# Optimization experiments

Measured on AMD Instinct MI355X. Metric: run time of the kernel, lower is better.

The kernel has to match this reference:

```python
import jax, jax.numpy as jnp
import numpy as np

EPS = 1e-6  # flax LayerNorm default

def _layernorm(x, scale, bias):
    mu = jnp.mean(x, axis=-1, keepdims=True)
    var = jnp.mean(jnp.square(x - mu), axis=-1, keepdims=True)
    return (x - mu) * jax.lax.rsqrt(var + EPS) * scale + bias

def _rel_pos_index(ws):
    coords = np.stack(np.meshgrid(np.arange(ws), np.arange(ws), indexing='ij'))  # [2,ws,ws]
    cf = coords.reshape(2, -1)
    rel = (cf[:, :, None] - cf[:, None, :]).transpose(1, 2, 0)  # [N,N,2]
    rel[..., 0] += ws - 1
    rel[..., 1] += ws - 1
    rel[..., 0] *= 2 * ws - 1
    return rel.sum(-1)  # [N,N] in [0,(2ws-1)^2)

def setup_inputs() -> dict:
    key = jax.random.key(0)
    ks = jax.random.split(key, 8)
    B, H, W, C = 16, 56, 56, 384
    L, heads, ws = 2, 12, 7
    s = 0.02
    return {
        'x': jax.random.normal(ks[0], (B, H, W, C), jnp.float32),
        'ln1_s': jnp.ones((L, C), jnp.float32),
        'ln1_b': jnp.zeros((L, C), jnp.float32),
        'qkv_w': jax.random.normal(ks[1], (L, C, 3 * C), jnp.float32) * s,
        'rpb': jax.random.normal(ks[2], (L, (2 * ws - 1) ** 2, heads), jnp.float32) * s,
        'proj_w': jax.random.normal(ks[3], (L, C, C), jnp.float32) * s,
        'ln2_s': jnp.ones((L, C), jnp.float32),
        'ln2_b': jnp.zeros((L, C), jnp.float32),
        'mlp_w1': jax.random.normal(ks[4], (L, C, 4 * C), jnp.float32) * s,
        'mlp_b1': jnp.zeros((L, 4 * C), jnp.float32),
        'mlp_w2': jax.random.normal(ks[5], (L, 4 * C, C), jnp.float32) * s,
        'mlp_b2': jnp.zeros((L, C), jnp.float32),
        'window_size': 7,
    }

def reference(x, ln1_s, ln1_b, qkv_w, rpb, proj_w, ln2_s, ln2_b, mlp_w1, mlp_b1, mlp_w2, mlp_b2, window_size):
    B, H, W, C = x.shape
    ws = int(window_size)
    L = qkv_w.shape[0]
    heads = rpb.shape[-1]
    hd = C // heads
    N = ws * ws
    idx = jnp.asarray(_rel_pos_index(ws))  # [N,N] static

    # --- split to windows: [B,H,W,C] -> [B*nWh*nWw, N, C]
    xw = x.reshape(B, H // ws, ws, W // ws, ws, C)
    xw = xw.transpose(0, 1, 3, 2, 4, 5).reshape(-1, N, C)

    for l in range(L):
        # --- windowed MHSA with relative position bias
        h = _layernorm(xw, ln1_s[l], ln1_b[l])
        qkv = (h @ qkv_w[l]).reshape(-1, N, 3, heads, hd)
        q, k, v = qkv[:, :, 0], qkv[:, :, 1], qkv[:, :, 2]  # [nW,N,heads,hd]
        attn = jnp.einsum('wqhd,wkhd->whqk', q, k) * (hd ** -0.5)
        bias = rpb[l][idx].transpose(2, 0, 1)  # [heads,N,N]
        attn = jax.nn.softmax(attn + bias[None], axis=-1)
        o = jnp.einsum('whqk,wkhd->wqhd', attn, v).reshape(-1, N, C)
        xw = xw + o @ proj_w[l]
        # --- MLP block
        h = _layernorm(xw, ln2_s[l], ln2_b[l])
        h = jax.nn.gelu(h @ mlp_w1[l] + mlp_b1[l])
        xw = xw + (h @ mlp_w2[l] + mlp_b2[l])

    # --- merge windows back to [B,H,W,C]
    out = xw.reshape(B, H // ws, W // ws, ws, ws, C)
    out = out.transpose(0, 1, 3, 2, 4, 5).reshape(B, H, W, C)
    return out
```

## Files before the change

### kernel.cpp

```cpp
#include <hip/hip_runtime.h>
#include <hip/hip_bf16.h>

typedef __bf16 bf16;
typedef __attribute__((ext_vector_type(4))) __bf16 bf16x4;
typedef __attribute__((ext_vector_type(8))) __bf16 bf16x8;
typedef __attribute__((ext_vector_type(4))) float f32x4;

__device__ __forceinline__ void async_ld16(const void* g, void* l) {
    __builtin_amdgcn_global_load_lds(
        (const __attribute__((address_space(1))) unsigned int*)g,
        (__attribute__((address_space(3))) unsigned int*)l, 16, 0, 0);
}

__global__ __launch_bounds__(256) void k_f2bt(const float* __restrict__ in,
                                              bf16* __restrict__ out, int Kd, int Nd) {
    int id = blockIdx.x * 256 + threadIdx.x;
    if (id >= Kd * Nd) return;
    int k = id / Nd, n = id - k * Nd;
    out[(size_t)n * Kd + k] = (bf16)in[id];
}

__global__ __launch_bounds__(256) void k_lnr(const float* __restrict__ x,
                                             const float* __restrict__ s,
                                             const float* __restrict__ b,
                                             float* __restrict__ xres,
                                             bf16* __restrict__ h) {
    int traw = blockIdx.x * 4 + (threadIdx.x >> 6);
    int lane = threadIdx.x & 63;
    int bb = traw / 3136;
    int rem = traw - bb * 3136;
    int y = rem / 56, xc = rem - y * 56;
    int w = bb * 64 + (y / 7) * 8 + (xc / 7);
    int n = (y % 7) * 7 + (xc % 7);
    int twin = w * 49 + n;

    const float4* row = (const float4*)(x + (size_t)traw * 384);
    float4 v0 = row[lane];
    float4 v1 = make_float4(0.f, 0.f, 0.f, 0.f);
    if (lane < 32) v1 = row[64 + lane];
    float sum = v0.x + v0.y + v0.z + v0.w + v1.x + v1.y + v1.z + v1.w;
#pragma unroll
    for (int m = 1; m < 64; m <<= 1) sum += __shfl_xor(sum, m);
    float mu = sum * (1.f / 384.f);
    float sq = (v0.x - mu) * (v0.x - mu) + (v0.y - mu) * (v0.y - mu) +
               (v0.z - mu) * (v0.z - mu) + (v0.w - mu) * (v0.w - mu);
    if (lane < 32)
        sq += (v1.x - mu) * (v1.x - mu) + (v1.y - mu) * (v1.y - mu) +
              (v1.z - mu) * (v1.z - mu) + (v1.w - mu) * (v1.w - mu);
#pragma unroll
    for (int m = 1; m < 64; m <<= 1) sq += __shfl_xor(sq, m);
    float r = rsqrtf(sq * (1.f / 384.f) + 1e-6f);

    float4* xr = (float4*)(xres + (size_t)twin * 384);
    const float4* s4 = (const float4*)s;
    const float4* b4 = (const float4*)b;
    bf16* ho = h + (size_t)twin * 384;
    {
        xr[lane] = v0;
        float4 sv = s4[lane], bv = b4[lane];
        bf16x4 ov;
        ov[0] = (bf16)((v0.x - mu) * r * sv.x + bv.x);
        ov[1] = (bf16)((v0.y - mu) * r * sv.y + bv.y);
        ov[2] = (bf16)((v0.z - mu) * r * sv.z + bv.z);
        ov[3] = (bf16)((v0.w - mu) * r * sv.w + bv.w);
        *(bf16x4*)&ho[lane * 4] = ov;
    }
    if (lane < 32) {
        xr[64 + lane] = v1;
        float4 sv = s4[64 + lane], bv = b4[64 + lane];
        bf16x4 ov;
        ov[0] = (bf16)((v1.x - mu) * r * sv.x + bv.x);
        ov[1] = (bf16)((v1.y - mu) * r * sv.y + bv.y);
        ov[2] = (bf16)((v1.z - mu) * r * sv.z + bv.z);
        ov[3] = (bf16)((v1.w - mu) * r * sv.w + bv.w);
        *(bf16x4*)&ho[256 + lane * 4] = ov;
    }
}

__global__ __launch_bounds__(256) void k_ln(const float* __restrict__ xres,
                                            const float* __restrict__ s,
                                            const float* __restrict__ b,
                                            bf16* __restrict__ h) {
    int t = blockIdx.x * 4 + (threadIdx.x >> 6);
    int lane = threadIdx.x & 63;
    const float4* row = (const float4*)(xres + (size_t)t * 384);
    float4 v0 = row[lane];
    float4 v1 = make_float4(0.f, 0.f, 0.f, 0.f);
    if (lane < 32) v1 = row[64 + lane];
    float sum = v0.x + v0.y + v0.z + v0.w + v1.x + v1.y + v1.z + v1.w;
#pragma unroll
    for (int m = 1; m < 64; m <<= 1) sum += __shfl_xor(sum, m);
    float mu = sum * (1.f / 384.f);
    float sq = (v0.x - mu) * (v0.x - mu) + (v0.y - mu) * (v0.y - mu) +
               (v0.z - mu) * (v0.z - mu) + (v0.w - mu) * (v0.w - mu);
    if (lane < 32)
        sq += (v1.x - mu) * (v1.x - mu) + (v1.y - mu) * (v1.y - mu) +
              (v1.z - mu) * (v1.z - mu) + (v1.w - mu) * (v1.w - mu);
#pragma unroll
    for (int m = 1; m < 64; m <<= 1) sq += __shfl_xor(sq, m);
    float r = rsqrtf(sq * (1.f / 384.f) + 1e-6f);
    const float4* s4 = (const float4*)s;
    const float4* b4 = (const float4*)b;
    bf16* ho = h + (size_t)t * 384;
    {
        float4 sv = s4[lane], bv = b4[lane];
        bf16x4 ov;
        ov[0] = (bf16)((v0.x - mu) * r * sv.x + bv.x);
        ov[1] = (bf16)((v0.y - mu) * r * sv.y + bv.y);
        ov[2] = (bf16)((v0.z - mu) * r * sv.z + bv.z);
        ov[3] = (bf16)((v0.w - mu) * r * sv.w + bv.w);
        *(bf16x4*)&ho[lane * 4] = ov;
    }
    if (lane < 32) {
        float4 sv = s4[64 + lane], bv = b4[64 + lane];
        bf16x4 ov;
        ov[0] = (bf16)((v1.x - mu) * r * sv.x + bv.x);
        ov[1] = (bf16)((v1.y - mu) * r * sv.y + bv.y);
        ov[2] = (bf16)((v1.z - mu) * r * sv.z + bv.z);
        ov[3] = (bf16)((v1.w - mu) * r * sv.w + bv.w);
        *(bf16x4*)&ho[256 + lane * 4] = ov;
    }
}

__device__ inline float gelu_f(float x) {
    float u = 0.7978845608028654f * (x + 0.044715f * x * x * x);
    float t = 1.f - 2.f / (__expf(2.f * u) + 1.f);
    return 0.5f * x * (1.f + t);
}

template <int EPI>
__global__ __launch_bounds__(256) void k_gemm(const bf16* __restrict__ A,
                                              const bf16* __restrict__ Bt,
                                              const float* __restrict__ bias,
                                              float* __restrict__ resid,
                                              bf16* __restrict__ Cout,
                                              float* __restrict__ outf,
                                              int N, int K) {
    __shared__ __align__(16) char lds[17408];
    bf16* As = (bf16*)lds;
    bf16* Bs = (bf16*)(lds + 8192);
    int tid = threadIdx.x;
    int n0 = blockIdx.x * 128;
    int m0 = blockIdx.y * 128;
    int wave = tid >> 6, lane = tid & 63;
    int wm = (wave >> 1) * 64, wn = (wave & 1) * 64;
    int col = lane & 15, quad = lane >> 4;

    f32x4 acc[4][4] = {};

    int r0 = 2 * wave * 16 + (lane >> 2);
    int ksl = (lane & 3) ^ ((r0 >> 1) & 3);
    const bf16* ga0 = A + (size_t)(m0 + r0) * K + ksl * 8;
    const bf16* gb0 = Bt + (size_t)(n0 + r0) * K + ksl * 8;
    size_t rowK16 = (size_t)16 * K;
    bf16* la0 = &As[2 * wave * 512];
    bf16* la1 = &As[(2 * wave + 1) * 512];
    bf16* lb0 = &Bs[2 * wave * 512];
    bf16* lb1 = &Bs[(2 * wave + 1) * 512];

    for (int kb = 0; kb < K; kb += 32) {
        __syncthreads();
        async_ld16(ga0 + kb, la0);
        async_ld16(ga0 + rowK16 + kb, la1);
        async_ld16(gb0 + kb, lb0);
        async_ld16(gb0 + rowK16 + kb, lb1);
        __syncthreads();

        bf16x8 af[4], bfv[4];
#pragma unroll
        for (int i = 0; i < 4; i++) {
            int ra = wm + i * 16 + col;
            af[i] = *(const bf16x8*)&As[ra * 32 + ((quad ^ ((ra >> 1) & 3)) << 3)];
            int rb = wn + i * 16 + col;
            bfv[i] = *(const bf16x8*)&Bs[rb * 32 + ((quad ^ ((rb >> 1) & 3)) << 3)];
        }
#pragma unroll
        for (int mi = 0; mi < 4; mi++)
#pragma unroll
            for (int ni = 0; ni < 4; ni++)
                acc[mi][ni] = __builtin_amdgcn_mfma_f32_16x16x32_bf16(
                    af[mi], bfv[ni], acc[mi][ni], 0, 0, 0);
    }

    __syncthreads();
    float* scrw = (float*)lds + wave * (16 * 68);

    int prow = lane >> 3;
    int pc0 = (lane & 7) * 8;
#pragma unroll
    for (int mi = 0; mi < 4; mi++) {
#pragma unroll
        for (int ni = 0; ni < 4; ni++)
#pragma unroll
            for (int r = 0; r < 4; r++)
                scrw[(quad * 4 + r) * 68 + ni * 16 + col] = acc[mi][ni][r];
#pragma unroll
        for (int h = 0; h < 2; h++) {
            int lr = h * 8 + prow;
            const float* sp = scrw + lr * 68 + pc0;
            float4 u0 = *(const float4*)sp;
            float4 u1 = *(const float4*)(sp + 4);
            int gm = m0 + wm + mi * 16 + lr;
            int gn = n0 + wn + pc0;
            size_t off = (size_t)gm * N + gn;
            if (EPI == 0) {
                bf16x8 ov;
                ov[0] = (bf16)u0.x; ov[1] = (bf16)u0.y; ov[2] = (bf16)u0.z; ov[3] = (bf16)u0.w;
                ov[4] = (bf16)u1.x; ov[5] = (bf16)u1.y; ov[6] = (bf16)u1.z; ov[7] = (bf16)u1.w;
                *(bf16x8*)&Cout[off] = ov;
            } else if (EPI == 1) {
                float4 b0 = *(const float4*)&bias[gn];
                float4 b1 = *(const float4*)&bias[gn + 4];
                bf16x8 ov;
                ov[0] = (bf16)gelu_f(u0.x + b0.x); ov[1] = (bf16)gelu_f(u0.y + b0.y);
                ov[2] = (bf16)gelu_f(u0.z + b0.z); ov[3] = (bf16)gelu_f(u0.w + b0.w);
                ov[4] = (bf16)gelu_f(u1.x + b1.x); ov[5] = (bf16)gelu_f(u1.y + b1.y);
                ov[6] = (bf16)gelu_f(u1.z + b1.z); ov[7] = (bf16)gelu_f(u1.w + b1.w);
                *(bf16x8*)&Cout[off] = ov;
            } else if (EPI == 2) {
                float4 r0v = *(const float4*)&resid[off];
                float4 r1v = *(const float4*)&resid[off + 4];
                r0v.x += u0.x; r0v.y += u0.y; r0v.z += u0.z; r0v.w += u0.w;
                r1v.x += u1.x; r1v.y += u1.y; r1v.z += u1.z; r1v.w += u1.w;
                *(float4*)&resid[off] = r0v;
                *(float4*)&resid[off + 4] = r1v;
            } else if (EPI == 3) {
                float4 b0 = *(const float4*)&bias[gn];
                float4 b1 = *(const float4*)&bias[gn + 4];
                float4 r0v = *(const float4*)&resid[off];
                float4 r1v = *(const float4*)&resid[off + 4];
                r0v.x += u0.x + b0.x; r0v.y += u0.y + b0.y;
                r0v.z += u0.z + b0.z; r0v.w += u0.w + b0.w;
                r1v.x += u1.x + b1.x; r1v.y += u1.y + b1.y;
                r1v.z += u1.z + b1.z; r1v.w += u1.w + b1.w;
                *(float4*)&resid[off] = r0v;
                *(float4*)&resid[off + 4] = r1v;
            } else {
                float4 b0 = *(const float4*)&bias[gn];
                float4 b1 = *(const float4*)&bias[gn + 4];
                float4 r0v = *(const float4*)&resid[off];
                float4 r1v = *(const float4*)&resid[off + 4];
                r0v.x += u0.x + b0.x; r0v.y += u0.y + b0.y;
                r0v.z += u0.z + b0.z; r0v.w += u0.w + b0.w;
                r1v.x += u1.x + b1.x; r1v.y += u1.y + b1.y;
                r1v.z += u1.z + b1.z; r1v.w += u1.w + b1.w;
                int wdx = gm / 49, n = gm - wdx * 49;
                int bb = wdx >> 6, r64 = wdx & 63;
                int n7 = n / 7;
                int yy = (r64 >> 3) * 7 + n7;
                int xx = (r64 & 7) * 7 + (n - n7 * 7);
                size_t traw = ((size_t)((bb * 56 + yy) * 56 + xx)) * 384 + gn;
                *(float4*)&outf[traw] = r0v;
                *(float4*)&outf[traw + 4] = r1v;
            }
        }
    }
}

__global__ __launch_bounds__(256) void k_attn(const bf16* __restrict__ qkv,
                                              const float* __restrict__ rpb,
                                              bf16* __restrict__ o) {
    __shared__ unsigned short relIdx[2401];
    __shared__ float rpbs[4][169];
    __shared__ __align__(16) bf16 Vs[4][32 * 72];
    __shared__ __align__(16) bf16 Ps[4][64 * 72];

    int tid = threadIdx.x;
    int wave = tid >> 6, lane = tid & 63;
    int col = lane & 15, quad = lane >> 4;
    int w = blockIdx.x;
    int head = blockIdx.y * 4 + wave;
    const float scale = 0.17677669529663687f;

    for (int e = tid; e < 2401; e += 256) {
        int i = e / 49, j = e - i * 49;
        int yi = i / 7, xi = i - yi * 7, yj = j / 7, xj = j - yj * 7;
        relIdx[e] = (unsigned short)((yi - yj + 6) * 13 + (xi - xj + 6));
    }
    for (int e = lane; e < 169; e += 64) rpbs[wave][e] = rpb[e * 12 + head];

    const bf16* base = qkv + (size_t)w * 49 * 1152 + head * 32;
    bf16* vsw = Vs[wave];
    bf16* psw = Ps[wave];

    bf16x4 z4 = {(bf16)0.f, (bf16)0.f, (bf16)0.f, (bf16)0.f};
    for (int e = lane; e < 576; e += 64) *(bf16x4*)&vsw[e * 4] = z4;
    for (int e = lane; e < 392; e += 64) {
        int j = e >> 3, d4 = (e & 7) * 4;
        bf16x4 vv = *(const bf16x4*)&base[768 + (size_t)j * 1152 + d4];
        vsw[(d4 + 0) * 72 + j] = vv[0];
        vsw[(d4 + 1) * 72 + j] = vv[1];
        vsw[(d4 + 2) * 72 + j] = vv[2];
        vsw[(d4 + 3) * 72 + j] = vv[3];
    }

    __syncthreads();

    bf16x8 qf[4], kf[4];
#pragma unroll
    for (int mi = 0; mi < 4; mi++) {
        size_t row = (size_t)(mi * 16 + col) * 1152 + quad * 8;
        qf[mi] = *(const bf16x8*)&base[row];
        kf[mi] = *(const bf16x8*)&base[384 + row];
    }

    f32x4 S[4][4] = {};
#pragma unroll
    for (int mi = 0; mi < 4; mi++)
#pragma unroll
        for (int nj = 0; nj < 4; nj++)
            S[mi][nj] = __builtin_amdgcn_mfma_f32_16x16x32_bf16(qf[mi], kf[nj], S[mi][nj], 0, 0, 0);

    float* rp = rpbs[wave];
#pragma unroll
    for (int mi = 0; mi < 4; mi++) {
#pragma unroll
        for (int r = 0; r < 4; r++) {
            int ii = mi * 16 + quad * 4 + r;
            int ir = (ii < 49 ? ii : 0) * 49;
            float sv[4];
            float mx = -1e30f;
#pragma unroll
            for (int nj = 0; nj < 4; nj++) {
                int j = nj * 16 + col;
                float v;
                if (j < 49) v = S[mi][nj][r] * scale + rp[relIdx[ir + j]];
                else v = -1e30f;
                sv[nj] = v;
                mx = fmaxf(mx, v);
            }
#pragma unroll
            for (int m = 1; m < 16; m <<= 1) mx = fmaxf(mx, __shfl_xor(mx, m));
            float sum = 0.f;
#pragma unroll
            for (int nj = 0; nj < 4; nj++) {
                float p = __expf(sv[nj] - mx);
                sv[nj] = p;
                sum += p;
            }
#pragma unroll
            for (int m = 1; m < 16; m <<= 1) sum += __shfl_xor(sum, m);
            float is = 1.f / sum;
#pragma unroll
            for (int nj = 0; nj < 4; nj++)
                psw[ii * 72 + nj * 16 + col] = (bf16)(sv[nj] * is);
        }
    }

    __syncthreads();

    f32x4 O[4][2] = {};
#pragma unroll
    for (int kt = 0; kt < 2; kt++) {
        bf16x8 vb[2];
#pragma unroll
        for (int nt = 0; nt < 2; nt++)
            vb[nt] = *(const bf16x8*)&vsw[(nt * 16 + col) * 72 + kt * 32 + quad * 8];
#pragma unroll
        for (int mi = 0; mi < 4; mi++) {
            bf16x8 pa = *(const bf16x8*)&psw[(mi * 16 + col) * 72 + kt * 32 + quad * 8];
#pragma unroll
            for (int nt = 0; nt < 2; nt++)
                O[mi][nt] = __builtin_amdgcn_mfma_f32_16x16x32_bf16(pa, vb[nt], O[mi][nt], 0, 0, 0);
        }
    }

    bf16* ob = o + (size_t)w * 49 * 384 + head * 32;
#pragma unroll
    for (int mi = 0; mi < 4; mi++) {
#pragma unroll
        for (int r = 0; r < 4; r++) {
            int i = mi * 16 + quad * 4 + r;
            if (i < 49) {
#pragma unroll
                for (int nt = 0; nt < 2; nt++)
                    ob[(size_t)i * 384 + nt * 16 + col] = (bf16)O[mi][nt][r];
            }
        }
    }
}

extern "C" void kernel_launch(void* const* d_in, const int* in_sizes, int n_in,
                              void* d_out, int out_size, void* d_ws, size_t ws_size,
                              hipStream_t stream) {
    const float* x      = (const float*)d_in[0];
    const float* ln1_s  = (const float*)d_in[1];
    const float* ln1_b  = (const float*)d_in[2];
    const float* qkv_w  = (const float*)d_in[3];
    const float* rpb    = (const float*)d_in[4];
    const float* proj_w = (const float*)d_in[5];
    const float* ln2_s  = (const float*)d_in[6];
    const float* ln2_b  = (const float*)d_in[7];
    const float* mlp_w1 = (const float*)d_in[8];
    const float* mlp_b1 = (const float*)d_in[9];
    const float* mlp_w2 = (const float*)d_in[10];
    const float* mlp_b2 = (const float*)d_in[11];
    float* out = (float*)d_out;

    char* ws = (char*)d_ws;
    float* xres  = (float*)ws;
    bf16* qkvbuf = (bf16*)(ws + 77070336);
    bf16* obuf   = (bf16*)(ws + 192675840);
    bf16* wbuf   = (bf16*)(ws + 231211008);
    bf16* hidden = qkvbuf;
    bf16* hbuf   = (bf16*)d_out;

    bf16* qkvw_b  = wbuf;
    bf16* projw_b = wbuf + 884736;
    bf16* mlp1_b  = wbuf + 1179648;
    bf16* mlp2_b  = wbuf + 2359296;

    for (int l = 0; l < 2; l++) {
        k_f2bt<<<1728, 256, 0, stream>>>(qkv_w + (size_t)l * 442368,
                                         qkvw_b + (size_t)l * 442368, 384, 1152);
        k_f2bt<<<576, 256, 0, stream>>>(proj_w + (size_t)l * 147456,
                                        projw_b + (size_t)l * 147456, 384, 384);
        k_f2bt<<<2304, 256, 0, stream>>>(mlp_w1 + (size_t)l * 589824,
                                         mlp1_b + (size_t)l * 589824, 384, 1536);
        k_f2bt<<<2304, 256, 0, stream>>>(mlp_w2 + (size_t)l * 589824,
                                         mlp2_b + (size_t)l * 589824, 1536, 384);
    }

    k_lnr<<<12544, 256, 0, stream>>>(x, ln1_s, ln1_b, xres, hbuf);

    for (int l = 0; l < 2; l++) {
        k_gemm<0><<<dim3(9, 392), 256, 0, stream>>>(
            hbuf, qkvw_b + (size_t)l * 442368, nullptr, nullptr, qkvbuf, nullptr, 1152, 384);
        k_attn<<<dim3(1024, 3), 256, 0, stream>>>(qkvbuf, rpb + l * 2028, obuf);
        k_gemm<2><<<dim3(3, 392), 256, 0, stream>>>(
            obuf, projw_b + (size_t)l * 147456, nullptr, xres, nullptr, nullptr, 384, 384);
        k_ln<<<12544, 256, 0, stream>>>(xres, ln2_s + l * 384, ln2_b + l * 384, hbuf);
        k_gemm<1><<<dim3(12, 392), 256, 0, stream>>>(
            hbuf, mlp1_b + (size_t)l * 589824, mlp_b1 + l * 1536, nullptr, hidden, nullptr, 1536, 384);
        if (l == 0) {
            k_gemm<3><<<dim3(3, 392), 256, 0, stream>>>(
                hidden, mlp2_b, mlp_b2, xres, nullptr, nullptr, 384, 1536);
            k_ln<<<12544, 256, 0, stream>>>(xres, ln1_s + 384, ln1_b + 384, hbuf);
        } else {
            k_gemm<4><<<dim3(3, 392), 256, 0, stream>>>(
                hidden, mlp2_b + 589824, mlp_b2 + 384, xres, nullptr, out, 384, 1536);
        }
    }
}
```

Before: 1.208 ms.

## Triple-buffer GEMM LDS tiles with async prefetch and manual vmcnt waits

Replaces the single-buffered K loop in the GEMM kernel with a three-stage LDS ring. Tiles are prefetched three steps ahead through global_load_lds, and completion is tracked with explicit vmcnt waits plus s_barrier. The aim is to hide global memory latency behind the MFMA work instead of stalling on two barriers each step. LDS per block grows from 17 KB to 48 KB, which can reduce occupancy. The hand-written waitcnt logic is fragile if the compiler reorders or adds memory ops.

```diff
diff --git a/kernel.cpp b/kernel.cpp
--- a/kernel.cpp
+++ b/kernel.cpp
@@ -136,9 +136,7 @@
                                               bf16* __restrict__ Cout,
                                               float* __restrict__ outf,
                                               int N, int K) {
-    __shared__ __align__(16) char lds[17408];
-    bf16* As = (bf16*)lds;
-    bf16* Bs = (bf16*)(lds + 8192);
+    __shared__ __align__(16) char lds[49152];
     int tid = threadIdx.x;
     int n0 = blockIdx.x * 128;
     int m0 = blockIdx.y * 128;
@@ -153,33 +151,56 @@
     const bf16* ga0 = A + (size_t)(m0 + r0) * K + ksl * 8;
     const bf16* gb0 = Bt + (size_t)(n0 + r0) * K + ksl * 8;
     size_t rowK16 = (size_t)16 * K;
-    bf16* la0 = &As[2 * wave * 512];
-    bf16* la1 = &As[(2 * wave + 1) * 512];
-    bf16* lb0 = &Bs[2 * wave * 512];
-    bf16* lb1 = &Bs[(2 * wave + 1) * 512];
-
-    for (int kb = 0; kb < K; kb += 32) {
-        __syncthreads();
-        async_ld16(ga0 + kb, la0);
-        async_ld16(ga0 + rowK16 + kb, la1);
-        async_ld16(gb0 + kb, lb0);
-        async_ld16(gb0 + rowK16 + kb, lb1);
-        __syncthreads();
-
+    int ldsoff = 2 * wave * 512;
+
+    int NT = K >> 5;
+
+    auto stage = [&](int t, int b) {
+        const bf16* a = ga0 + t * 32;
+        const bf16* g = gb0 + t * 32;
+        char* base = (char*)lds + b * 16384;
+        bf16* Ab = (bf16*)base;
+        bf16* Bb = (bf16*)(base + 8192);
+        async_ld16(a, Ab + ldsoff);
+        async_ld16(a + rowK16, Ab + ldsoff + 512);
+        async_ld16(g, Bb + ldsoff);
+        async_ld16(g + rowK16, Bb + ldsoff + 512);
+    };
+
+    stage(0, 0);
+    stage(1, 1);
+    stage(2, 2);
+
+    int buf = 0;
+    for (int t = 0; t < NT; ++t) {
+        int rem = NT - 1 - t;
+        if (rem >= 2)
+            asm volatile("s_waitcnt vmcnt(8)\n\ts_barrier" ::: "memory");
+        else if (rem == 1)
+            asm volatile("s_waitcnt vmcnt(4)\n\ts_barrier" ::: "memory");
+        else
+            asm volatile("s_waitcnt vmcnt(0)\n\ts_barrier" ::: "memory");
+
+        const char* base = (const char*)lds + buf * 16384;
+        const bf16* Ab = (const bf16*)base;
+        const bf16* Bb = (const bf16*)(base + 8192);
         bf16x8 af[4], bfv[4];
 #pragma unroll
         for (int i = 0; i < 4; i++) {
             int ra = wm + i * 16 + col;
-            af[i] = *(const bf16x8*)&As[ra * 32 + ((quad ^ ((ra >> 1) & 3)) << 3)];
+            af[i] = *(const bf16x8*)&Ab[ra * 32 + ((quad ^ ((ra >> 1) & 3)) << 3)];
             int rb = wn + i * 16 + col;
-            bfv[i] = *(const bf16x8*)&Bs[rb * 32 + ((quad ^ ((rb >> 1) & 3)) << 3)];
-        }
+            bfv[i] = *(const bf16x8*)&Bb[rb * 32 + ((quad ^ ((rb >> 1) & 3)) << 3)];
+        }
+        asm volatile("s_waitcnt lgkmcnt(0)\n\ts_barrier" ::: "memory");
+        if (t + 3 < NT) stage(t + 3, buf);
 #pragma unroll
         for (int mi = 0; mi < 4; mi++)
 #pragma unroll
             for (int ni = 0; ni < 4; ni++)
                 acc[mi][ni] = __builtin_amdgcn_mfma_f32_16x16x32_bf16(
                     af[mi], bfv[ni], acc[mi][ni], 0, 0, 0);
+        buf = (buf == 2) ? 0 : buf + 1;
     }
 
     __syncthreads();
```

Result: faster. 1.135 ms (-6.0%).
